# Kernel optimization log

Measured on AMD Instinct MI355X. Metric: run time of the kernel, lower is better.

Reference implementation:

```python
import jax, jax.numpy as jnp
import numpy as np

B, D, H, W, L = 32, 768, 14, 14, 77
TEMP_G, TEMP1, TEMP2, TEMP3 = 10.0, 4.0, 5.0, 10.0
LAMBDA_G, LAMBDA_L = 1.0, 1.0
EPS = 1e-8
NEG = -1e30


def setup_inputs() -> dict:
    key = jax.random.key(0)
    k1, k2, k3, k4, k5 = jax.random.split(key, 5)
    img_global = jax.random.normal(k1, (B, D), dtype=jnp.float32)
    img_local = jax.random.normal(k2, (B, D, H, W), dtype=jnp.float32)
    text_global = jax.random.normal(k3, (B, D), dtype=jnp.float32)
    text_local = jax.random.normal(k4, (B, L, D), dtype=jnp.float32)
    # ragged caption lengths: prefix attention mask, lengths in [10, L]
    lens = jax.random.randint(k5, (B,), 10, L + 1)
    attention_mask = (jnp.arange(L)[None, :] < lens[:, None]).astype(jnp.int32)
    return {"img_global": img_global, "img_local": img_local,
            "text_global": text_global, "text_local": text_local,
            "attention_mask": attention_mask}


def _ce_arange(scores):
    # cross entropy with labels = arange(n), mean reduction
    return jnp.mean(jax.nn.logsumexp(scores, axis=1) - jnp.diagonal(scores))


def _gloria_loss(img_global, img_local, text_global, text_local, attention_mask):
    mask = attention_mask.astype(bool)                      # [B, L]
    # ---- global contrastive loss ----
    in_ = img_global / jnp.maximum(jnp.linalg.norm(img_global, axis=1, keepdims=True), 1e-12)
    tn_ = text_global / jnp.maximum(jnp.linalg.norm(text_global, axis=1, keepdims=True), 1e-12)
    g_scores = (in_ @ tn_.T) * TEMP_G                       # [B, B]
    loss_global = 0.5 * (_ce_arange(g_scores) + _ce_arange(g_scores.T))

    # ---- local contrastive loss (vectorized over all text/image pairs) ----
    tl = jnp.swapaxes(text_local, 1, 2)                     # [B, D, L] (forward() transposes since L != D)
    ctx = img_local.reshape(B, D, H * W)                    # [B, D, S]
    # raw attention logits: text i words vs image j pixels -> [i, j, s, l]
    logits = jnp.einsum('jds,idl->ijsl', ctx, tl)
    logits = jnp.where(mask[:, None, None, :], logits, NEG)
    a1 = jax.nn.softmax(logits, axis=-1)                    # softmax over words (first softmax)
    a2 = jax.nn.softmax(TEMP1 * jnp.swapaxes(a1, 2, 3), axis=-1)  # [i, j, l, s], softmax over pixels
    wctx = jnp.einsum('jds,ijls->ijdl', ctx, a2)            # weighted context [i, j, D, l]
    # cosine similarity per word, over feature dim
    w12 = jnp.einsum('idl,ijdl->ijl', tl, wctx)
    n1 = jnp.linalg.norm(tl, axis=1)                        # [i, l]
    n2 = jnp.linalg.norm(wctx, axis=2)                      # [i, j, l]
    cos = w12 / jnp.maximum(n1[:, None, :] * n2, EPS)       # [i, j, l]
    row = jnp.exp(TEMP2 * cos) * mask[:, None, :]           # mask padded words
    sim = jnp.log(row.sum(axis=-1))                         # [i, j]  (local_agg='sum')
    # torch cats per-caption columns: similarities[j, i] -> transpose
    scores = sim.T * TEMP3                                  # [img j, text i]
    loss_local = 0.5 * (_ce_arange(scores) + _ce_arange(scores.T))

    return LAMBDA_G * loss_global + LAMBDA_L * loss_local


def reference(img_global, img_local, text_global, text_local, attention_mask):
    return _gloria_loss(img_global, img_local, text_global, text_local, attention_mask)
```

## Files before the change

kernel.cpp:

```cpp
#include <hip/hip_runtime.h>
#include <math.h>

#define NB 32
#define ND 768
#define NS 196
#define NL 77

typedef _Float16 f16x8 __attribute__((ext_vector_type(8)));
typedef float f32x4 __attribute__((ext_vector_type(4)));

__device__ __forceinline__ f32x4 mfma16(f16x8 a, f16x8 b, f32x4 c) {
  return __builtin_amdgcn_mfma_f32_16x16x32_f16(a, b, c, 0, 0, 0);
}

#define GLOAD16(gp, lp)                                          \
  __builtin_amdgcn_global_load_lds(                              \
      (const __attribute__((address_space(1))) void*)(gp),       \
      (__attribute__((address_space(3))) void*)(lp), 16, 0, 0)


__global__ __launch_bounds__(256) void prep_all_kernel(
    const float* __restrict__ text_local,
    const float* __restrict__ img_local,
    const int* __restrict__ amask,
    _Float16* __restrict__ txf, _Float16* __restrict__ cTf,
    float* __restrict__ n1ws, int* __restrict__ lenws) {
  const int bid = blockIdx.x;
  const int t = threadIdx.x;
  __shared__ float tile[32][213];

  if (bid < 960) {
    int tau = bid * 256 + t;
    int i = tau / 7680;
    int r = tau - i * 7680;
    int dk = r / 320;
    int r2 = r - dk * 320;
    int lt = r2 >> 6, lane = r2 & 63;
    int n16 = lane & 15, g = lane >> 4;
    int l = lt * 16 + n16;
    float v[8];
#pragma unroll
    for (int q = 0; q < 8; ++q) v[q] = 0.f;
    if (l < NL) {
      const float* src = text_local + ((size_t)i * NL + l) * ND + dk * 32 + g * 8;
      float4 a = *(const float4*)src;
      float4 b = *(const float4*)(src + 4);
      v[0] = a.x; v[1] = a.y; v[2] = a.z; v[3] = a.w;
      v[4] = b.x; v[5] = b.y; v[6] = b.z; v[7] = b.w;
    }
    f16x8 hv;
#pragma unroll
    for (int q = 0; q < 8; ++q) hv[q] = (_Float16)v[q];
    size_t base = (((size_t)i * 24 + dk) * 5 + lt) * 512 + (size_t)lane * 8;
    *(f16x8*)(txf + base) = hv;
  } else if (bid < 1344) {
    const int b2 = bid - 960;
    const int j = b2 / 12, dc = b2 - (b2 / 12) * 12;
    const float* src = img_local + ((size_t)j * ND + dc * 64) * NS;
#pragma unroll 1
    for (int h = 0; h < 2; ++h) {
      __syncthreads();
      for (int idx = t; idx < 1568; idx += 256) {
        int dd = idx / 49, sq = idx - dd * 49;
        float4 v = *(const float4*)(src + (size_t)(h * 32 + dd) * NS + sq * 4);
        tile[dd][sq * 4 + 0] = v.x;
        tile[dd][sq * 4 + 1] = v.y;
        tile[dd][sq * 4 + 2] = v.z;
        tile[dd][sq * 4 + 3] = v.w;
      }
      __syncthreads();
      const int dk = dc * 2 + h;
      for (int idx = t; idx < 832; idx += 256) {
        int lane = idx & 63;
        int S = idx >> 6;
        int n16 = lane & 15, g = lane >> 4;
        int s = S * 16 + n16;
        f16x8 hv;
#pragma unroll
        for (int e = 0; e < 8; ++e) {
          float v = (s < NS) ? tile[g * 8 + e][s] : 0.f;
          hv[e] = (_Float16)v;
        }
        size_t base = (((size_t)j * 13 + S) * 24 + dk) * 512 + (size_t)lane * 8;
        *(f16x8*)(cTf + base) = hv;
      }
    }
  } else {
    const int i = bid - 1344;
    const int lane = t & 63, w = t >> 6;
    __shared__ int slen;
    if (t == 0) slen = 0;
    __syncthreads();
    if (t < NL && amask[i * NL + t] != 0) atomicAdd(&slen, 1);
    for (int l = w; l < NL; l += 4) {
      const float4* p = (const float4*)(text_local + ((size_t)i * NL + l) * ND);
      float s = 0.f;
#pragma unroll
      for (int k = 0; k < 3; ++k) {
        float4 v = p[lane + 64 * k];
        s += v.x * v.x + v.y * v.y + v.z * v.z + v.w * v.w;
      }
#pragma unroll
      for (int off = 32; off; off >>= 1) s += __shfl_xor(s, off);
      if (lane == 0) n1ws[i * 80 + l] = sqrtf(s);
    }
    __syncthreads();
    if (t == 0) lenws[i] = slen;
  }
}

__global__ void mid_kernel(const _Float16* __restrict__ cTf, _Float16* __restrict__ Gf,
                           const float* __restrict__ img_global,
                           const float* __restrict__ text_global,
                           float* __restrict__ gscw,
                           const int* __restrict__ lenws, int* __restrict__ ordws) {
  const int bid = blockIdx.x;
  const int t = threadIdx.x;
  __shared__ __align__(16) float shi[ND];

  if (bid < 832) {
    const int j = bid / 26;
    const int rr = bid - j * 26;
    const int st = rr >> 1, ch = rr & 1;
    const int lane = t & 63, w = t >> 6;
    const int g = lane >> 4, n16 = lane & 15;
    const f32x4 z4 = {0.f, 0.f, 0.f, 0.f};
    f32x4 accG[2];
    accG[0] = z4; accG[1] = z4;
    const int base = ch * 7;
    const int ncols = ch ? 6 : 7;
    const size_t cj = (size_t)j * 13;
    for (int dk = 0; dk < 24; ++dk) {
      size_t ao = ((cj + st) * 24 + dk) * 512 + (size_t)lane * 8;
      f16x8 A = *(const f16x8*)(cTf + ao);
#pragma unroll
      for (int q = 0; q < 2; ++q) {
        int ntl = w + (q << 2);
        if (ntl < ncols) {
          int nt = base + ntl;
          size_t bo = ((cj + nt) * 24 + dk) * 512 + (size_t)lane * 8;
          f16x8 B = *(const f16x8*)(cTf + bo);
          accG[q] = mfma16(A, B, accG[q]);
        }
      }
    }
#pragma unroll
    for (int q = 0; q < 2; ++q) {
      int ntl = w + (q << 2);
      int nt = base + ntl;
      bool compute = (ntl < ncols);
      bool zfill = (ch == 1 && nt == 13);
      if (compute || zfill) {
#pragma unroll
        for (int r = 0; r < 4; ++r) {
          int col = nt * 16 + n16;
          float v = compute ? accG[q][r] : 0.f;
          int kt = col >> 5, gg = (col >> 3) & 3, e = col & 7;
          int lane2 = (g * 4 + r) + (gg << 4);
          size_t o = (((size_t)j * 13 + st) * 7 + kt) * 512 + (size_t)lane2 * 8 + e;
          Gf[o] = (_Float16)v;
        }
      }
    }
  } else if (bid < 864) {
    const int a = bid - 832;
    const int lane = t & 63, w = t >> 6;
    if (t < ND / 4) ((float4*)shi)[t] = ((const float4*)(img_global + (size_t)a * ND))[t];
    __syncthreads();
    for (int b = w; b < NB; b += 4) {
      const float4* pt = (const float4*)(text_global + (size_t)b * ND);
      const float4* pi = (const float4*)shi;
      float dot = 0.f, ni = 0.f, nt = 0.f;
#pragma unroll
      for (int k = 0; k < 3; ++k) {
        float4 x = pi[lane + 64 * k];
        float4 y = pt[lane + 64 * k];
        dot += x.x * y.x + x.y * y.y + x.z * y.z + x.w * y.w;
        ni  += x.x * x.x + x.y * x.y + x.z * x.z + x.w * x.w;
        nt  += y.x * y.x + y.y * y.y + y.z * y.z + y.w * y.w;
      }
#pragma unroll
      for (int off = 32; off; off >>= 1) {
        dot += __shfl_xor(dot, off);
        ni  += __shfl_xor(ni, off);
        nt  += __shfl_xor(nt, off);
      }
      if (lane == 0)
        gscw[a * NB + b] = dot / fmaxf(sqrtf(ni), 1e-12f) / fmaxf(sqrtf(nt), 1e-12f) * 10.0f;
    }
  } else {
    if (t == 0) {
      int o[32];
      for (int k = 0; k < 32; ++k) o[k] = k;
      for (int x = 0; x < 31; ++x) {
        int best = x;
        for (int y = x + 1; y < 32; ++y)
          if (lenws[o[y]] > lenws[o[best]]) best = y;
        int tmp = o[x]; o[x] = o[best]; o[best] = tmp;
      }
      for (int k = 0; k < 32; ++k) ordws[k] = o[k];
    }
  }
}

__global__ __launch_bounds__(512, 3) void pair_kernel(
    const _Float16* __restrict__ txf, const _Float16* __restrict__ cTf,
    const _Float16* __restrict__ Gf,
    const float* __restrict__ n1ws, const int* __restrict__ lenws,
    const int* __restrict__ ordws,
    float* __restrict__ simws) {
  const int t = threadIdx.x;
  const int wg = ((blockIdx.x & 7) << 6) + (blockIdx.x >> 3);
  const int j = wg >> 4;
  const int m = wg & 15;
  const int i0 = ordws[m], i1 = ordws[31 - m];
  const int len0 = lenws[i0], len1 = lenws[i1];
  const int nlt0 = (len0 + 15) >> 4, nlt1 = (len1 + 15) >> 4;
  const int lane = t & 63, wid = t >> 6;
  const int g = lane >> 4, n16 = lane & 15;
  const bool vb = (wid < 5);

  __shared__ __align__(16) union {
    _Float16 e2f[7 * 5 * 64 * 8];
    _Float16 b1[2][2][2][5][512];
  } U;
  __shared__ float w12s[80], z2s[80], n2s[80];

  const f32x4 z4 = {0.f, 0.f, 0.f, 0.f};
  f32x4 acc[2][2][5];
#pragma unroll
  for (int p = 0; p < 2; ++p)
#pragma unroll
    for (int q = 0; q < 2; ++q)
#pragma unroll
      for (int lt = 0; lt < 5; ++lt) acc[p][q][lt] = z4;

  const _Float16* txi0 = txf + (size_t)i0 * 24 * 5 * 512;
  const _Float16* txi1 = txf + (size_t)i1 * 24 * 5 * 512;
  const size_t cj = (size_t)j * 13;
  const int c0 = (wid < 5) ? wid : (wid - 5);

  GLOAD16(txi0 + ((size_t)(0 * 5 + c0) << 9) + ((size_t)lane << 3), &U.b1[0][0][0][c0][0]);
  GLOAD16(txi1 + ((size_t)(0 * 5 + c0) << 9) + ((size_t)lane << 3), &U.b1[0][0][1][c0][0]);
  GLOAD16(txi0 + ((size_t)(1 * 5 + c0) << 9) + ((size_t)lane << 3), &U.b1[0][1][0][c0][0]);
  GLOAD16(txi1 + ((size_t)(1 * 5 + c0) << 9) + ((size_t)lane << 3), &U.b1[0][1][1][c0][0]);
  __syncthreads();

#pragma unroll 1
  for (int dkp = 0; dkp < 12; ++dkp) {
    const int cur = dkp & 1;
    const int dk0 = dkp * 2;
    f16x8 Aa0, Ab0, Aa1, Ab1;
    {
      size_t ao = ((cj + wid) * 24 + dk0) * 512 + ((size_t)lane << 3);
      Aa0 = *(const f16x8*)(cTf + ao);
      Aa1 = *(const f16x8*)(cTf + ao + 512);
    }
    if (vb) {
      size_t ao = ((cj + wid + 8) * 24 + dk0) * 512 + ((size_t)lane << 3);
      Ab0 = *(const f16x8*)(cTf + ao);
      Ab1 = *(const f16x8*)(cTf + ao + 512);
    }
    if (dkp < 11) {
      GLOAD16(txi0 + ((size_t)((dk0 + 2) * 5 + c0) << 9) + ((size_t)lane << 3),
              &U.b1[cur ^ 1][0][0][c0][0]);
      GLOAD16(txi1 + ((size_t)((dk0 + 2) * 5 + c0) << 9) + ((size_t)lane << 3),
              &U.b1[cur ^ 1][0][1][c0][0]);
      GLOAD16(txi0 + ((size_t)((dk0 + 3) * 5 + c0) << 9) + ((size_t)lane << 3),
              &U.b1[cur ^ 1][1][0][c0][0]);
      GLOAD16(txi1 + ((size_t)((dk0 + 3) * 5 + c0) << 9) + ((size_t)lane << 3),
              &U.b1[cur ^ 1][1][1][c0][0]);
    }
    __builtin_amdgcn_s_setprio(1);
#pragma unroll
    for (int lt = 0; lt < 5; ++lt) {
      if (lt < nlt0) {
        f16x8 B0 = *(const f16x8*)&U.b1[cur][0][0][lt][lane << 3];
        acc[0][0][lt] = mfma16(Aa0, B0, acc[0][0][lt]);
        if (vb) acc[0][1][lt] = mfma16(Ab0, B0, acc[0][1][lt]);
      }
      if (lt < nlt1) {
        f16x8 B1 = *(const f16x8*)&U.b1[cur][0][1][lt][lane << 3];
        acc[1][0][lt] = mfma16(Aa0, B1, acc[1][0][lt]);
        if (vb) acc[1][1][lt] = mfma16(Ab0, B1, acc[1][1][lt]);
      }
    }
#pragma unroll
    for (int lt = 0; lt < 5; ++lt) {
      if (lt < nlt0) {
        f16x8 B0 = *(const f16x8*)&U.b1[cur][1][0][lt][lane << 3];
        acc[0][0][lt] = mfma16(Aa1, B0, acc[0][0][lt]);
        if (vb) acc[0][1][lt] = mfma16(Ab1, B0, acc[0][1][lt]);
      }
      if (lt < nlt1) {
        f16x8 B1 = *(const f16x8*)&U.b1[cur][1][1][lt][lane << 3];
        acc[1][0][lt] = mfma16(Aa1, B1, acc[1][0][lt]);
        if (vb) acc[1][1][lt] = mfma16(Ab1, B1, acc[1][1][lt]);
      }
    }
    __builtin_amdgcn_s_setprio(0);
    __syncthreads();
  }

#pragma unroll
  for (int p = 0; p < 2; ++p) {
    const int ip   = p ? i1 : i0;
    const int lenp = p ? len1 : len0;
    const int nltp = p ? nlt1 : nlt0;

    __syncthreads();
    if (t < 80) { w12s[t] = 0.f; z2s[t] = 0.f; n2s[t] = 0.f; }
    for (int idx = t; idx < 2240; idx += 512)
      ((uint4*)U.e2f)[idx] = make_uint4(0, 0, 0, 0);
    __syncthreads();

    float w12loc[5], z2loc[5];
#pragma unroll
    for (int lt = 0; lt < 5; ++lt) { w12loc[lt] = 0.f; z2loc[lt] = 0.f; }
#pragma unroll
    for (int q = 0; q < 2; ++q) {
      const int S = wid + (q << 3);
      if (q == 0 || vb) {
#pragma unroll
        for (int r = 0; r < 4; ++r) {
          int s = S * 16 + g * 4 + r;
          bool srow = (s < NS);
          float mx = -1e30f;
#pragma unroll
          for (int lt = 0; lt < 5; ++lt) {
            if (lt < nltp) {
              if ((lt * 16 + n16) < lenp) mx = fmaxf(mx, acc[p][q][lt][r]);
            }
          }
          mx = fmaxf(mx, __shfl_xor(mx, 1));
          mx = fmaxf(mx, __shfl_xor(mx, 2));
          mx = fmaxf(mx, __shfl_xor(mx, 4));
          mx = fmaxf(mx, __shfl_xor(mx, 8));
          float z = 0.f;
          float ev[5];
#pragma unroll
          for (int lt = 0; lt < 5; ++lt) {
            float e = 0.f;
            if (lt < nltp) {
              if ((lt * 16 + n16) < lenp) e = __expf(acc[p][q][lt][r] - mx);
            }
            ev[lt] = e;
            z += e;
          }
          z += __shfl_xor(z, 1);
          z += __shfl_xor(z, 2);
          z += __shfl_xor(z, 4);
          z += __shfl_xor(z, 8);
          float inv = 4.0f / z;
#pragma unroll
          for (int lt = 0; lt < 5; ++lt) {
            if (lt < nltp) {
              if (((lt * 16 + n16) < lenp) && srow) {
                float e2 = __expf(ev[lt] * inv);
                w12loc[lt] += e2 * acc[p][q][lt][r];
                z2loc[lt] += e2;
                int kt = s >> 5, kk = s & 31;
                U.e2f[(((kt * 5) + lt) * 64 + (n16 + ((kk >> 3) << 4))) * 8 + (kk & 7)] = (_Float16)e2;
              }
            }
          }
        }
      }
    }
#pragma unroll
    for (int lt = 0; lt < 5; ++lt) {
      w12loc[lt] += __shfl_xor(w12loc[lt], 16);
      w12loc[lt] += __shfl_xor(w12loc[lt], 32);
      z2loc[lt] += __shfl_xor(z2loc[lt], 16);
      z2loc[lt] += __shfl_xor(z2loc[lt], 32);
    }
    if (lane < 16) {
#pragma unroll
      for (int lt = 0; lt < 5; ++lt) {
        if (lt < nltp) {
          atomicAdd(&w12s[lt * 16 + lane], w12loc[lt]);
          atomicAdd(&z2s[lt * 16 + lane], z2loc[lt]);
        }
      }
    }
    __syncthreads();

    float n2loc[5];
#pragma unroll
    for (int lt = 0; lt < 5; ++lt) n2loc[lt] = 0.f;
#pragma unroll
    for (int q = 0; q < 2; ++q) {
      const int S = wid + (q << 3);
      if (q == 0 || vb) {
        f32x4 a2[5];
#pragma unroll
        for (int lt = 0; lt < 5; ++lt) a2[lt] = z4;
        const _Float16* gp = Gf + (((size_t)j * 13 + S) * 7) * 512 + ((size_t)lane << 3);
        f16x8 GA = *(const f16x8*)gp;
#pragma unroll
        for (int kt = 0; kt < 7; ++kt) {
          f16x8 GAN;
          if (kt < 6) GAN = *(const f16x8*)(gp + (size_t)(kt + 1) * 512);
          __builtin_amdgcn_s_setprio(1);
#pragma unroll
          for (int lt = 0; lt < 5; ++lt) {
            if (lt < nltp) {
              f16x8 Bv = *(const f16x8*)&U.e2f[(((kt * 5) + lt) * 64 + lane) * 8];
              a2[lt] = mfma16(GA, Bv, a2[lt]);
            }
          }
          __builtin_amdgcn_s_setprio(0);
          if (kt < 6) GA = GAN;
        }
#pragma unroll
        for (int lt = 0; lt < 5; ++lt) {
          if (lt < nltp) {
#pragma unroll
            for (int r = 0; r < 4; ++r) {
              int s = S * 16 + g * 4 + r;
              int kt = s >> 5, kk = s & 31;
              float e2v = (float)U.e2f[(((kt * 5) + lt) * 64 + (n16 + ((kk >> 3) << 4))) * 8 + (kk & 7)];
              n2loc[lt] += e2v * a2[lt][r];
            }
          }
        }
      }
    }
#pragma unroll
    for (int lt = 0; lt < 5; ++lt) {
      n2loc[lt] += __shfl_xor(n2loc[lt], 16);
      n2loc[lt] += __shfl_xor(n2loc[lt], 32);
    }
    if (lane < 16) {
#pragma unroll
      for (int lt = 0; lt < 5; ++lt) {
        if (lt < nltp) atomicAdd(&n2s[lt * 16 + lane], n2loc[lt]);
      }
    }
    __syncthreads();

    if (t < lenp) {
      float z2 = z2s[t];
      float w12v = w12s[t] / z2;
      float n2v = sqrtf(n2s[t]) / z2;
      float n1v = n1ws[ip * 80 + t];
      float cosv = w12v / fmaxf(n1v * n2v, 1e-8f);
      w12s[t] = __expf(5.0f * cosv);
    }
    __syncthreads();
    if (wid == 0) {
      float e = (lane < lenp) ? w12s[lane] : 0.f;
      if (lane + 64 < lenp) e += w12s[lane + 64];
      e += __shfl_xor(e, 1);
      e += __shfl_xor(e, 2);
      e += __shfl_xor(e, 4);
      e += __shfl_xor(e, 8);
      e += __shfl_xor(e, 16);
      e += __shfl_xor(e, 32);
      if (lane == 0) simws[ip * NB + j] = __logf(e);
    }
  }
}

__global__ void loss_kernel(const float* __restrict__ gscw,
                            const float* __restrict__ simws,
                            float* __restrict__ out) {
  const int t = threadIdx.x;
  __shared__ float gs[NB][NB];
  __shared__ float sl[NB][NB];
  __shared__ float parts[4][NB];
  {
    float4 gv = ((const float4*)gscw)[t];
    ((float4*)gs)[t] = gv;
    float4 v = ((const float4*)simws)[t];
    int ii = t >> 3;
    int j0 = (t & 7) * 4;
    sl[j0 + 0][ii] = v.x * 10.0f;
    sl[j0 + 1][ii] = v.y * 10.0f;
    sl[j0 + 2][ii] = v.z * 10.0f;
    sl[j0 + 3][ii] = v.w * 10.0f;
  }
  __syncthreads();
  if (t < NB) {
    float m, z;
    m = -1e30f;
    for (int c = 0; c < NB; ++c) m = fmaxf(m, gs[t][c]);
    z = 0.f;
    for (int c = 0; c < NB; ++c) z += __expf(gs[t][c] - m);
    parts[0][t] = m + __logf(z) - gs[t][t];

    m = -1e30f;
    for (int c = 0; c < NB; ++c) m = fmaxf(m, gs[c][t]);
    z = 0.f;
    for (int c = 0; c < NB; ++c) z += __expf(gs[c][t] - m);
    parts[1][t] = m + __logf(z) - gs[t][t];

    m = -1e30f;
    for (int c = 0; c < NB; ++c) m = fmaxf(m, sl[t][c]);
    z = 0.f;
    for (int c = 0; c < NB; ++c) z += __expf(sl[t][c] - m);
    parts[2][t] = m + __logf(z) - sl[t][t];

    m = -1e30f;
    for (int c = 0; c < NB; ++c) m = fmaxf(m, sl[c][t]);
    z = 0.f;
    for (int c = 0; c < NB; ++c) z += __expf(sl[c][t] - m);
    parts[3][t] = m + __logf(z) - sl[t][t];
  }
  __syncthreads();
  if (t == 0) {
    float s0 = 0.f, s1 = 0.f, s2 = 0.f, s3 = 0.f;
    for (int r = 0; r < NB; ++r) {
      s0 += parts[0][r]; s1 += parts[1][r];
      s2 += parts[2][r]; s3 += parts[3][r];
    }
    out[0] = 0.5f * (s0 + s1) / 32.0f + 0.5f * (s2 + s3) / 32.0f;
  }
}

extern "C" void kernel_launch(void* const* d_in, const int* in_sizes, int n_in,
                              void* d_out, int out_size, void* d_ws, size_t ws_size,
                              hipStream_t stream) {
  (void)in_sizes; (void)n_in; (void)out_size; (void)ws_size;
  const float* img_global  = (const float*)d_in[0];
  const float* img_local   = (const float*)d_in[1];
  const float* text_global = (const float*)d_in[2];
  const float* text_local  = (const float*)d_in[3];
  const int*   amask       = (const int*)d_in[4];

  _Float16* txf = (_Float16*)d_ws;
  _Float16* cTf = txf + (size_t)1966080;
  _Float16* Gf  = cTf + (size_t)5111808;
  float* fsm  = (float*)(Gf + (size_t)1490944);
  float* n1ws  = fsm;
  float* simws = fsm + 2560;
  float* gscw  = fsm + 3584;
  int*   lenws = (int*)(fsm + 4608);
  int*   ordws = (int*)(fsm + 4640);

  prep_all_kernel<<<1376, 256, 0, stream>>>(text_local, img_local, amask,
                                            txf, cTf, n1ws, lenws);
  mid_kernel<<<865, 256, 0, stream>>>(cTf, Gf, img_global, text_global,
                                      gscw, lenws, ordws);
  pair_kernel<<<512, 512, 0, stream>>>(txf, cTf, Gf, n1ws, lenws, ordws, simws);
  loss_kernel<<<1, 256, 0, stream>>>(gscw, simws, (float*)d_out);
}
```

Baseline: 118.3 us.

## Use 1024-thread pair blocks with one pixel tile per wave

Widens the pair kernel from 512 to 1024 threads so each of 13 active waves owns a single 16-pixel tile, instead of 8 waves each covering up to two tiles. The text-tile staging into LDS is redistributed across 20 wave slots. The goal is to cut per-wave serial MFMA and softmax work and registers, raising parallelism per block. In exchange, three of the sixteen waves sit idle and occupancy is capped at two blocks per CU, with more threads taking part in each barrier.

```diff
diff --git a/kernel.cpp b/kernel.cpp
--- a/kernel.cpp
+++ b/kernel.cpp
@@ -203,7 +203,7 @@
   }
 }
 
-__global__ __launch_bounds__(512, 3) void pair_kernel(
+__global__ __launch_bounds__(1024, 2) void pair_kernel(
     const _Float16* __restrict__ txf, const _Float16* __restrict__ cTf,
     const _Float16* __restrict__ Gf,
     const float* __restrict__ n1ws, const int* __restrict__ lenws,
@@ -218,7 +218,7 @@
   const int nlt0 = (len0 + 15) >> 4, nlt1 = (len1 + 15) >> 4;
   const int lane = t & 63, wid = t >> 6;
   const int g = lane >> 4, n16 = lane & 15;
-  const bool vb = (wid < 5);
+  const bool va = (wid < 13);
 
   __shared__ __align__(16) union {
     _Float16 e2f[7 * 5 * 64 * 8];
@@ -227,75 +227,68 @@
   __shared__ float w12s[80], z2s[80], n2s[80];
 
   const f32x4 z4 = {0.f, 0.f, 0.f, 0.f};
-  f32x4 acc[2][2][5];
+  f32x4 acc[2][5];
 #pragma unroll
   for (int p = 0; p < 2; ++p)
 #pragma unroll
-    for (int q = 0; q < 2; ++q)
-#pragma unroll
-      for (int lt = 0; lt < 5; ++lt) acc[p][q][lt] = z4;
+    for (int lt = 0; lt < 5; ++lt) acc[p][lt] = z4;
 
   const _Float16* txi0 = txf + (size_t)i0 * 24 * 5 * 512;
   const _Float16* txi1 = txf + (size_t)i1 * 24 * 5 * 512;
   const size_t cj = (size_t)j * 13;
-  const int c0 = (wid < 5) ? wid : (wid - 5);
-
-  GLOAD16(txi0 + ((size_t)(0 * 5 + c0) << 9) + ((size_t)lane << 3), &U.b1[0][0][0][c0][0]);
-  GLOAD16(txi1 + ((size_t)(0 * 5 + c0) << 9) + ((size_t)lane << 3), &U.b1[0][0][1][c0][0]);
-  GLOAD16(txi0 + ((size_t)(1 * 5 + c0) << 9) + ((size_t)lane << 3), &U.b1[0][1][0][c0][0]);
-  GLOAD16(txi1 + ((size_t)(1 * 5 + c0) << 9) + ((size_t)lane << 3), &U.b1[0][1][1][c0][0]);
+
+#define STAGE(BUF, DKBASE)                                                       \
+  do {                                                                           \
+    _Pragma("unroll")                                                            \
+    for (int k = 0; k < 2; ++k) {                                                \
+      int slot = wid + (k << 4);                                                 \
+      if (slot < 20) {                                                           \
+        int d = slot / 10, rem = slot - d * 10;                                  \
+        int ii = rem / 5, lt = rem - ii * 5;                                     \
+        const _Float16* tx = ii ? txi1 : txi0;                                   \
+        GLOAD16(tx + ((size_t)(((DKBASE) + d) * 5 + lt) << 9) + ((size_t)lane << 3), \
+                &U.b1[BUF][d][ii][lt][0]);                                       \
+      }                                                                          \
+    }                                                                            \
+  } while (0)
+
+  STAGE(0, 0);
   __syncthreads();
 
 #pragma unroll 1
   for (int dkp = 0; dkp < 12; ++dkp) {
     const int cur = dkp & 1;
     const int dk0 = dkp * 2;
-    f16x8 Aa0, Ab0, Aa1, Ab1;
-    {
+    f16x8 Aa0, Aa1;
+    if (va) {
       size_t ao = ((cj + wid) * 24 + dk0) * 512 + ((size_t)lane << 3);
       Aa0 = *(const f16x8*)(cTf + ao);
       Aa1 = *(const f16x8*)(cTf + ao + 512);
     }
-    if (vb) {
-      size_t ao = ((cj + wid + 8) * 24 + dk0) * 512 + ((size_t)lane << 3);
-      Ab0 = *(const f16x8*)(cTf + ao);
-      Ab1 = *(const f16x8*)(cTf + ao + 512);
-    }
-    if (dkp < 11) {
-      GLOAD16(txi0 + ((size_t)((dk0 + 2) * 5 + c0) << 9) + ((size_t)lane << 3),
-              &U.b1[cur ^ 1][0][0][c0][0]);
-      GLOAD16(txi1 + ((size_t)((dk0 + 2) * 5 + c0) << 9) + ((size_t)lane << 3),
-              &U.b1[cur ^ 1][0][1][c0][0]);
-      GLOAD16(txi0 + ((size_t)((dk0 + 3) * 5 + c0) << 9) + ((size_t)lane << 3),
-              &U.b1[cur ^ 1][1][0][c0][0]);
-      GLOAD16(txi1 + ((size_t)((dk0 + 3) * 5 + c0) << 9) + ((size_t)lane << 3),
-              &U.b1[cur ^ 1][1][1][c0][0]);
-    }
+    if (dkp < 11) STAGE(cur ^ 1, dk0 + 2);
     __builtin_amdgcn_s_setprio(1);
-#pragma unroll
-    for (int lt = 0; lt < 5; ++lt) {
-      if (lt < nlt0) {
-        f16x8 B0 = *(const f16x8*)&U.b1[cur][0][0][lt][lane << 3];
-        acc[0][0][lt] = mfma16(Aa0, B0, acc[0][0][lt]);
-        if (vb) acc[0][1][lt] = mfma16(Ab0, B0, acc[0][1][lt]);
-      }
-      if (lt < nlt1) {
-        f16x8 B1 = *(const f16x8*)&U.b1[cur][0][1][lt][lane << 3];
-        acc[1][0][lt] = mfma16(Aa0, B1, acc[1][0][lt]);
-        if (vb) acc[1][1][lt] = mfma16(Ab0, B1, acc[1][1][lt]);
-      }
-    }
-#pragma unroll
-    for (int lt = 0; lt < 5; ++lt) {
-      if (lt < nlt0) {
-        f16x8 B0 = *(const f16x8*)&U.b1[cur][1][0][lt][lane << 3];
-        acc[0][0][lt] = mfma16(Aa1, B0, acc[0][0][lt]);
-        if (vb) acc[0][1][lt] = mfma16(Ab1, B0, acc[0][1][lt]);
-      }
-      if (lt < nlt1) {
-        f16x8 B1 = *(const f16x8*)&U.b1[cur][1][1][lt][lane << 3];
-        acc[1][0][lt] = mfma16(Aa1, B1, acc[1][0][lt]);
-        if (vb) acc[1][1][lt] = mfma16(Ab1, B1, acc[1][1][lt]);
+    if (va) {
+#pragma unroll
+      for (int lt = 0; lt < 5; ++lt) {
+        if (lt < nlt0) {
+          f16x8 B0 = *(const f16x8*)&U.b1[cur][0][0][lt][lane << 3];
+          acc[0][lt] = mfma16(Aa0, B0, acc[0][lt]);
+        }
+        if (lt < nlt1) {
+          f16x8 B1 = *(const f16x8*)&U.b1[cur][0][1][lt][lane << 3];
+          acc[1][lt] = mfma16(Aa0, B1, acc[1][lt]);
+        }
+      }
+#pragma unroll
+      for (int lt = 0; lt < 5; ++lt) {
+        if (lt < nlt0) {
+          f16x8 B0 = *(const f16x8*)&U.b1[cur][1][0][lt][lane << 3];
+          acc[0][lt] = mfma16(Aa1, B0, acc[0][lt]);
+        }
+        if (lt < nlt1) {
+          f16x8 B1 = *(const f16x8*)&U.b1[cur][1][1][lt][lane << 3];
+          acc[1][lt] = mfma16(Aa1, B1, acc[1][lt]);
+        }
       }
     }
     __builtin_amdgcn_s_setprio(0);
@@ -310,58 +303,55 @@
 
     __syncthreads();
     if (t < 80) { w12s[t] = 0.f; z2s[t] = 0.f; n2s[t] = 0.f; }
-    for (int idx = t; idx < 2240; idx += 512)
+    for (int idx = t; idx < 2240; idx += 1024)
       ((uint4*)U.e2f)[idx] = make_uint4(0, 0, 0, 0);
     __syncthreads();
 
     float w12loc[5], z2loc[5];
 #pragma unroll
     for (int lt = 0; lt < 5; ++lt) { w12loc[lt] = 0.f; z2loc[lt] = 0.f; }
-#pragma unroll
-    for (int q = 0; q < 2; ++q) {
-      const int S = wid + (q << 3);
-      if (q == 0 || vb) {
-#pragma unroll
-        for (int r = 0; r < 4; ++r) {
-          int s = S * 16 + g * 4 + r;
-          bool srow = (s < NS);
-          float mx = -1e30f;
-#pragma unroll
-          for (int lt = 0; lt < 5; ++lt) {
-            if (lt < nltp) {
-              if ((lt * 16 + n16) < lenp) mx = fmaxf(mx, acc[p][q][lt][r]);
-            }
+    if (va) {
+      const int S = wid;
+#pragma unroll
+      for (int r = 0; r < 4; ++r) {
+        int s = S * 16 + g * 4 + r;
+        bool srow = (s < NS);
+        float mx = -1e30f;
+#pragma unroll
+        for (int lt = 0; lt < 5; ++lt) {
+          if (lt < nltp) {
+            if ((lt * 16 + n16) < lenp) mx = fmaxf(mx, acc[p][lt][r]);
           }
-          mx = fmaxf(mx, __shfl_xor(mx, 1));
-          mx = fmaxf(mx, __shfl_xor(mx, 2));
-          mx = fmaxf(mx, __shfl_xor(mx, 4));
-          mx = fmaxf(mx, __shfl_xor(mx, 8));
-          float z = 0.f;
-          float ev[5];
-#pragma unroll
-          for (int lt = 0; lt < 5; ++lt) {
-            float e = 0.f;
-            if (lt < nltp) {
-              if ((lt * 16 + n16) < lenp) e = __expf(acc[p][q][lt][r] - mx);
-            }
-            ev[lt] = e;
-            z += e;
+        }
+        mx = fmaxf(mx, __shfl_xor(mx, 1));
+        mx = fmaxf(mx, __shfl_xor(mx, 2));
+        mx = fmaxf(mx, __shfl_xor(mx, 4));
+        mx = fmaxf(mx, __shfl_xor(mx, 8));
+        float z = 0.f;
+        float ev[5];
+#pragma unroll
+        for (int lt = 0; lt < 5; ++lt) {
+          float e = 0.f;
+          if (lt < nltp) {
+            if ((lt * 16 + n16) < lenp) e = __expf(acc[p][lt][r] - mx);
           }
-          z += __shfl_xor(z, 1);
-          z += __shfl_xor(z, 2);
-          z += __shfl_xor(z, 4);
-          z += __shfl_xor(z, 8);
-          float inv = 4.0f / z;
-#pragma unroll
-          for (int lt = 0; lt < 5; ++lt) {
-            if (lt < nltp) {
-              if (((lt * 16 + n16) < lenp) && srow) {
-                float e2 = __expf(ev[lt] * inv);
-                w12loc[lt] += e2 * acc[p][q][lt][r];
-                z2loc[lt] += e2;
-                int kt = s >> 5, kk = s & 31;
-                U.e2f[(((kt * 5) + lt) * 64 + (n16 + ((kk >> 3) << 4))) * 8 + (kk & 7)] = (_Float16)e2;
-              }
+          ev[lt] = e;
+          z += e;
+        }
+        z += __shfl_xor(z, 1);
+        z += __shfl_xor(z, 2);
+        z += __shfl_xor(z, 4);
+        z += __shfl_xor(z, 8);
+        float inv = 4.0f / z;
+#pragma unroll
+        for (int lt = 0; lt < 5; ++lt) {
+          if (lt < nltp) {
+            if (((lt * 16 + n16) < lenp) && srow) {
+              float e2 = __expf(ev[lt] * inv);
+              w12loc[lt] += e2 * acc[p][lt][r];
+              z2loc[lt] += e2;
+              int kt = s >> 5, kk = s & 31;
+              U.e2f[(((kt * 5) + lt) * 64 + (n16 + ((kk >> 3) << 4))) * 8 + (kk & 7)] = (_Float16)e2;
             }
           }
         }
@@ -374,7 +364,7 @@
       z2loc[lt] += __shfl_xor(z2loc[lt], 16);
       z2loc[lt] += __shfl_xor(z2loc[lt], 32);
     }
-    if (lane < 16) {
+    if (va && lane < 16) {
 #pragma unroll
       for (int lt = 0; lt < 5; ++lt) {
         if (lt < nltp) {
@@ -388,40 +378,37 @@
     float n2loc[5];
 #pragma unroll
     for (int lt = 0; lt < 5; ++lt) n2loc[lt] = 0.f;
-#pragma unroll
-    for (int q = 0; q < 2; ++q) {
-      const int S = wid + (q << 3);
-      if (q == 0 || vb) {
-        f32x4 a2[5];
-#pragma unroll
-        for (int lt = 0; lt < 5; ++lt) a2[lt] = z4;
-        const _Float16* gp = Gf + (((size_t)j * 13 + S) * 7) * 512 + ((size_t)lane << 3);
-        f16x8 GA = *(const f16x8*)gp;
-#pragma unroll
-        for (int kt = 0; kt < 7; ++kt) {
-          f16x8 GAN;
-          if (kt < 6) GAN = *(const f16x8*)(gp + (size_t)(kt + 1) * 512);
-          __builtin_amdgcn_s_setprio(1);
-#pragma unroll
-          for (int lt = 0; lt < 5; ++lt) {
-            if (lt < nltp) {
-              f16x8 Bv = *(const f16x8*)&U.e2f[(((kt * 5) + lt) * 64 + lane) * 8];
-              a2[lt] = mfma16(GA, Bv, a2[lt]);
-            }
-          }
-          __builtin_amdgcn_s_setprio(0);
-          if (kt < 6) GA = GAN;
-        }
+    if (va) {
+      const int S = wid;
+      f32x4 a2[5];
+#pragma unroll
+      for (int lt = 0; lt < 5; ++lt) a2[lt] = z4;
+      const _Float16* gp = Gf + (((size_t)j * 13 + S) * 7) * 512 + ((size_t)lane << 3);
+      f16x8 GA = *(const f16x8*)gp;
+#pragma unroll
+      for (int kt = 0; kt < 7; ++kt) {
+        f16x8 GAN;
+        if (kt < 6) GAN = *(const f16x8*)(gp + (size_t)(kt + 1) * 512);
+        __builtin_amdgcn_s_setprio(1);
 #pragma unroll
         for (int lt = 0; lt < 5; ++lt) {
           if (lt < nltp) {
-#pragma unroll
-            for (int r = 0; r < 4; ++r) {
-              int s = S * 16 + g * 4 + r;
-              int kt = s >> 5, kk = s & 31;
-              float e2v = (float)U.e2f[(((kt * 5) + lt) * 64 + (n16 + ((kk >> 3) << 4))) * 8 + (kk & 7)];
-              n2loc[lt] += e2v * a2[lt][r];
-            }
+            f16x8 Bv = *(const f16x8*)&U.e2f[(((kt * 5) + lt) * 64 + lane) * 8];
+            a2[lt] = mfma16(GA, Bv, a2[lt]);
+          }
+        }
+        __builtin_amdgcn_s_setprio(0);
+        if (kt < 6) GA = GAN;
+      }
+#pragma unroll
+      for (int lt = 0; lt < 5; ++lt) {
+        if (lt < nltp) {
+#pragma unroll
+          for (int r = 0; r < 4; ++r) {
+            int s = S * 16 + g * 4 + r;
+            int kt = s >> 5, kk = s & 31;
+            float e2v = (float)U.e2f[(((kt * 5) + lt) * 64 + (n16 + ((kk >> 3) << 4))) * 8 + (kk & 7)];
+            n2loc[lt] += e2v * a2[lt][r];
           }
         }
       }
@@ -431,7 +418,7 @@
       n2loc[lt] += __shfl_xor(n2loc[lt], 16);
       n2loc[lt] += __shfl_xor(n2loc[lt], 32);
     }
-    if (lane < 16) {
+    if (va && lane < 16) {
 #pragma unroll
       for (int lt = 0; lt < 5; ++lt) {
         if (lt < nltp) atomicAdd(&n2s[lt * 16 + lane], n2loc[lt]);
@@ -460,6 +447,7 @@
       if (lane == 0) simws[ip * NB + j] = __logf(e);
     }
   }
+#undef STAGE
 }
 
 __global__ void loss_kernel(const float* __restrict__ gscw,
@@ -542,6 +530,6 @@
                                             txf, cTf, n1ws, lenws);
   mid_kernel<<<865, 256, 0, stream>>>(cTf, Gf, img_global, text_global,
                                       gscw, lenws, ordws);
-  pair_kernel<<<512, 512, 0, stream>>>(txf, cTf, Gf, n1ws, lenws, ordws, simws);
+  pair_kernel<<<512, 1024, 0, stream>>>(txf, cTf, Gf, n1ws, lenws, ordws, simws);
   loss_kernel<<<1, 256, 0, stream>>>(gscw, simws, (float*)d_out);
 }
```

After: 140.1 us. 18.3% more time.
